# Optimization experiments

Measured on AMD Instinct MI355X. Metric: run time of the kernel, lower is better.

Reference implementation:

```python
import jax, jax.numpy as jnp
import numpy as np

EMB = 512
HEADS = 8

def setup_inputs() -> dict:
    key = jax.random.key(0)
    ks = jax.random.split(key, 9)
    s = 1.0 / np.sqrt(EMB)
    x = jax.random.normal(ks[0], (32, 4096, EMB), dtype=jnp.float32)
    Wq = jax.random.normal(ks[1], (EMB, EMB), dtype=jnp.float32) * s
    bq = jax.random.normal(ks[2], (EMB,), dtype=jnp.float32) * s
    Wk = jax.random.normal(ks[3], (EMB, EMB), dtype=jnp.float32) * s
    bk = jax.random.normal(ks[4], (EMB,), dtype=jnp.float32) * s
    Wv = jax.random.normal(ks[5], (EMB, EMB), dtype=jnp.float32) * s
    bv = jax.random.normal(ks[6], (EMB,), dtype=jnp.float32) * s
    Wo = jax.random.normal(ks[7], (EMB, EMB), dtype=jnp.float32) * s
    bo = jax.random.normal(ks[8], (EMB,), dtype=jnp.float32) * s
    return {"x": x, "Wq": Wq, "bq": bq, "Wk": Wk, "bk": bk,
            "Wv": Wv, "bv": bv, "Wo": Wo, "bo": bo}

def reference(x, Wq, bq, Wk, bk, Wv, bv, Wo, bo):
    b, n, e = x.shape
    h = HEADS
    d = e // h
    scale = jnp.asarray(d ** 0.5, x.dtype)
    # torch Linear: y = x @ W.T + b
    q = (x @ Wq.T + bq).reshape(b, n, h, d)
    k = (x @ Wk.T + bk).reshape(b, n, h, d)
    v = (x @ Wv.T + bv).reshape(b, n, h, d)
    # NOTE: contracts over sequence axis n (faithful to original einsum),
    # producing a (b, h, d, d) feature-feature score matrix.
    qk = jnp.einsum('bnhq,bnhk->bhqk', q, k) / scale
    attn = jax.nn.softmax(qk, axis=-1)  # softmax over head_dim axis
    # dropout is identity at inference
    weighted = jnp.einsum('bhqk,bnhk->bnhq', attn, v).reshape(b, n, e)
    return weighted @ Wo.T + bo
```

## Files before the change

### kernel.cpp

```cpp
#include <hip/hip_runtime.h>
#include <hip/hip_bf16.h>
#include <stdint.h>

#define BATCH 32
#define SEQ   4096
#define EMB   512
#define HEADS 8
#define HD    64
#define SCALE 0.125f

typedef __attribute__((ext_vector_type(8))) short bf16x8;
typedef __attribute__((ext_vector_type(4))) float f32x4;

__device__ __forceinline__ unsigned short f2bf(float f) {
    union { float f; unsigned int u; } v; v.f = f;
    unsigned int u = v.u;
    return (unsigned short)((u + 0x7FFFu + ((u >> 16) & 1u)) >> 16);
}
__device__ __forceinline__ float bf2f(unsigned short h) {
    union { unsigned int u; float f; } v; v.u = ((unsigned int)h) << 16;
    return v.f;
}
__device__ __forceinline__ unsigned int cvtpk(float lo, float hi) {
    unsigned int r;
    asm("v_cvt_pk_bf16_f32 %0, %1, %2" : "=v"(r) : "v"(lo), "v"(hi));
    return r;
}
__device__ __forceinline__ float lo_as_f(unsigned int p) {
    union { unsigned int u; float f; } v; v.u = p << 16; return v.f;
}
__device__ __forceinline__ float hi_as_f(unsigned int p) {
    union { unsigned int u; float f; } v; v.u = p & 0xFFFF0000u; return v.f;
}

#define MFMA16(a, b, c) __builtin_amdgcn_mfma_f32_16x16x32_bf16((a), (b), (c), 0, 0, 0)

union F4 { float4 v; float f[4]; };
struct Regs { F4 a0, a1, a2, a3; };

template <int NCHUNK, bool XBF>
__global__ __launch_bounds__(1024) void k1_gram(const float* __restrict__ x,
                                                float* __restrict__ P,
                                                float* __restrict__ svp,
                                                unsigned short* __restrict__ xbf) {
  constexpr int KC  = SEQ / NCHUNK;
  constexpr int NIT = KC / 32;
  constexpr int NWG = BATCH * 4 * NCHUNK;
  constexpr int PER = NWG / 8;
  const int bid = blockIdx.x;
  const int wk  = (bid & 7) * PER + (bid >> 3);
  const int c   = (NCHUNK == 2) ? (wk & 1) : 0;
  const int tt  = (NCHUNK == 2) ? ((wk >> 1) & 3) : (wk & 3);
  const int b   = (NCHUNK == 2) ? (wk >> 3) : (wk >> 2);
  const int mt = (tt >> 1) & 1, nt = tt & 1;
  const int m0 = mt * 256, n0 = nt * 256;
  const bool diag = (mt == nt);
  const float* __restrict__ xb = x + (size_t)b * SEQ * EMB;
  const int kbeg = c * KC;

  __shared__ unsigned short L[2][64 * 148];
  __shared__ float SR[256][8];

  const int tid  = threadIdx.x;
  const int lane = tid & 63;
  const int wave = tid >> 6;
  const int wr = (wave >> 2) * 64;
  const int wc = (wave & 3) * 64;
  const int er  = lane & 15;
  const int kb8 = (lane >> 4) * 8;

  const int fg   = lane;
  const int kgrp = wave >> 1;
  const bool isB = (wave & 1);
  const int pcol = isB ? n0 : m0;
  const bool active = (!diag) || (!isB);

  f32x4 acc[4][4];
#pragma unroll
  for (int i = 0; i < 4; ++i)
#pragma unroll
    for (int j = 0; j < 4; ++j) acc[i][j] = (f32x4){0.f, 0.f, 0.f, 0.f};

  float sacc[4] = {0.f, 0.f, 0.f, 0.f};

  Regs r0;

  auto loadreg = [&](int t) {
    const float* p = &xb[(size_t)(kbeg + t * 32 + kgrp * 4) * EMB + pcol + fg * 4];
    r0.a0.v = *(const float4*)p;
    r0.a1.v = *(const float4*)(p + EMB);
    r0.a2.v = *(const float4*)(p + 2 * EMB);
    r0.a3.v = *(const float4*)(p + 3 * EMB);
  };

  auto stage = [&](int t) {
    unsigned short* __restrict__ Ld = &L[isB ? 1 : 0][0];
#pragma unroll
    for (int i = 0; i < 4; ++i) {
      uint2 w;
      w.x = cvtpk(r0.a0.f[i], r0.a1.f[i]);
      w.y = cvtpk(r0.a2.f[i], r0.a3.f[i]);
      *(uint2*)&Ld[fg * 148 + i * 36 + kgrp * 4] = w;
    }
    if (diag) {
#pragma unroll
      for (int i = 0; i < 4; ++i)
        sacc[i] += (r0.a0.f[i] + r0.a1.f[i]) + (r0.a2.f[i] + r0.a3.f[i]);
      if (XBF) {
        unsigned short* xp = &xbf[((size_t)b * SEQ + kbeg + t * 32 + kgrp * 4) * EMB + m0 + fg * 4];
        uint2 xr;
        xr.x = cvtpk(r0.a0.f[0], r0.a0.f[1]); xr.y = cvtpk(r0.a0.f[2], r0.a0.f[3]);
        *(uint2*)&xp[0] = xr;
        xr.x = cvtpk(r0.a1.f[0], r0.a1.f[1]); xr.y = cvtpk(r0.a1.f[2], r0.a1.f[3]);
        *(uint2*)&xp[EMB] = xr;
        xr.x = cvtpk(r0.a2.f[0], r0.a2.f[1]); xr.y = cvtpk(r0.a2.f[2], r0.a2.f[3]);
        *(uint2*)&xp[2 * EMB] = xr;
        xr.x = cvtpk(r0.a3.f[0], r0.a3.f[1]); xr.y = cvtpk(r0.a3.f[2], r0.a3.f[3]);
        *(uint2*)&xp[3 * EMB] = xr;
      }
    }
  };

  auto frag = [&](const unsigned short* __restrict__ Ls, int e) -> bf16x8 {
    const int off = (e >> 2) * 148 + (e & 3) * 36 + kb8;
    union { bf16x8 v; uint2 u[2]; } r;
    r.u[0] = *(const uint2*)&Ls[off];
    r.u[1] = *(const uint2*)&Ls[off + 4];
    return r.v;
  };

  if (active) loadreg(0);

  for (int it = 0; it < NIT; ++it) {
    __syncthreads();
    if (active) stage(it);
    __syncthreads();
    if (active && (it + 1 < NIT)) loadreg(it + 1);

    const unsigned short* __restrict__ LAs = &L[0][0];
    const unsigned short* __restrict__ LBs = diag ? LAs : &L[1][0];
    bf16x8 bfr[4];
#pragma unroll
    for (int ns = 0; ns < 4; ++ns) bfr[ns] = frag(LBs, wc + ns * 16 + er);
    {
      bf16x8 a0f = frag(LAs, wr + er);
      bf16x8 a1f = frag(LAs, wr + 16 + er);
#pragma unroll
      for (int ns = 0; ns < 4; ++ns) {
        acc[0][ns] = MFMA16(a0f, bfr[ns], acc[0][ns]);
        acc[1][ns] = MFMA16(a1f, bfr[ns], acc[1][ns]);
      }
    }
    {
      bf16x8 a2f = frag(LAs, wr + 32 + er);
      bf16x8 a3f = frag(LAs, wr + 48 + er);
#pragma unroll
      for (int ns = 0; ns < 4; ++ns) {
        acc[2][ns] = MFMA16(a2f, bfr[ns], acc[2][ns]);
        acc[3][ns] = MFMA16(a3f, bfr[ns], acc[3][ns]);
      }
    }
  }

  float* __restrict__ Pc = P + (size_t)(c * BATCH + b) * EMB * EMB;
#pragma unroll
  for (int ms = 0; ms < 4; ++ms)
#pragma unroll
    for (int ns = 0; ns < 4; ++ns)
#pragma unroll
      for (int r = 0; r < 4; ++r) {
        const int row = m0 + wr + ms * 16 + ((lane >> 4) * 4) + r;
        const int col = n0 + wc + ns * 16 + (lane & 15);
        Pc[(size_t)row * EMB + col] = acc[ms][ns][r];
      }

  if (diag) {
    __syncthreads();
    if (!isB) {
#pragma unroll
      for (int i = 0; i < 4; ++i) SR[fg * 4 + i][kgrp] = sacc[i];
    }
    __syncthreads();
    if (tid < 256) {
      float v = 0.f;
#pragma unroll
      for (int j = 0; j < 8; ++j) v += SR[tid][j];
      svp[(size_t)(c * BATCH + b) * EMB + m0 + tid] = v;
    }
  }
}

template <bool TWO>
__global__ __launch_bounds__(256) void k2a_wqg(const float* __restrict__ Wq,
                                               const float* __restrict__ P,
                                               float* __restrict__ A) {
  const int bid = blockIdx.x;
  const int wk  = (bid & 7) * 64 + (bid >> 3);
  const int b  = wk >> 4;
  const int mt = (wk >> 2) & 3;
  const int nt = wk & 3;
  const int m0 = mt * 128, n0 = nt * 128;
  const float* __restrict__ P0b = P + (size_t)b * EMB * EMB;
  const float* __restrict__ P1b = P + (size_t)(BATCH + b) * EMB * EMB;

  __shared__ unsigned short LA[128][40];
  __shared__ unsigned short LBhi[128][40];
  __shared__ unsigned short LBlo[128][40];

  const int tid  = threadIdx.x;
  const int lane = tid & 63;
  const int wave = tid >> 6;
  const int wr = (wave >> 1) * 64;
  const int wc = (wave & 1) * 64;

  f32x4 acc[4][4];
#pragma unroll
  for (int i = 0; i < 4; ++i)
#pragma unroll
    for (int j = 0; j < 4; ++j) acc[i][j] = (f32x4){0.f, 0.f, 0.f, 0.f};

  const int rA = tid >> 3, fgA = tid & 7;

  for (int k0 = 0; k0 < EMB; k0 += 32) {
    __syncthreads();
#pragma unroll
    for (int it = 0; it < 4; ++it) {
      const int r = rA + it * 32;
      const float4 v = *(const float4*)&Wq[(size_t)(m0 + r) * EMB + k0 + fgA * 4];
      uint2 u; u.x = cvtpk(v.x, v.y); u.y = cvtpk(v.z, v.w);
      *(uint2*)&LA[r][fgA * 4] = u;
    }
#pragma unroll
    for (int it = 0; it < 4; ++it) {
      const int r = rA + it * 32;
      float4 v = *(const float4*)&P0b[(size_t)(n0 + r) * EMB + k0 + fgA * 4];
      if (TWO) {
        const float4 v1 = *(const float4*)&P1b[(size_t)(n0 + r) * EMB + k0 + fgA * 4];
        v.x += v1.x; v.y += v1.y; v.z += v1.z; v.w += v1.w;
      }
      uint2 h; h.x = cvtpk(v.x, v.y); h.y = cvtpk(v.z, v.w);
      uint2 l;
      l.x = cvtpk(v.x - lo_as_f(h.x), v.y - hi_as_f(h.x));
      l.y = cvtpk(v.z - lo_as_f(h.y), v.w - hi_as_f(h.y));
      *(uint2*)&LBhi[r][fgA * 4] = h;
      *(uint2*)&LBlo[r][fgA * 4] = l;
    }
    __syncthreads();
    bf16x8 af[4], bh[4], bl[4];
#pragma unroll
    for (int ms = 0; ms < 4; ++ms)
      af[ms] = *(const bf16x8*)&LA[wr + ms*16 + (lane & 15)][(lane >> 4) * 8];
#pragma unroll
    for (int ns = 0; ns < 4; ++ns) {
      bh[ns] = *(const bf16x8*)&LBhi[wc + ns*16 + (lane & 15)][(lane >> 4) * 8];
      bl[ns] = *(const bf16x8*)&LBlo[wc + ns*16 + (lane & 15)][(lane >> 4) * 8];
    }
#pragma unroll
    for (int ms = 0; ms < 4; ++ms)
#pragma unroll
      for (int ns = 0; ns < 4; ++ns) {
        acc[ms][ns] = MFMA16(af[ms], bh[ns], acc[ms][ns]);
        acc[ms][ns] = MFMA16(af[ms], bl[ns], acc[ms][ns]);
      }
  }

  float* __restrict__ Ab = A + (size_t)b * EMB * EMB;
#pragma unroll
  for (int ms = 0; ms < 4; ++ms)
#pragma unroll
    for (int ns = 0; ns < 4; ++ns)
#pragma unroll
      for (int r = 0; r < 4; ++r) {
        const int row = m0 + wr + ms*16 + ((lane >> 4) * 4) + r;
        const int col = n0 + wc + ns*16 + (lane & 15);
        Ab[(size_t)row * EMB + col] = acc[ms][ns][r];
      }
}

template <int NCHUNK>
__global__ __launch_bounds__(256) void k2b_logits(const float* __restrict__ A,
                                                  const float* __restrict__ Wq,
                                                  const float* __restrict__ Wk,
                                                  const float* __restrict__ bq,
                                                  const float* __restrict__ bk,
                                                  const float* __restrict__ svp,
                                                  unsigned short* __restrict__ attn) {
  const int blk = blockIdx.x;
  const int b = blk >> 3;
  const int h = blk & 7;
  const float* __restrict__ Ab = A + (size_t)b * EMB * EMB + (size_t)h * HD * EMB;

  __shared__ unsigned short LAhi[64][40];
  __shared__ unsigned short LAlo[64][40];
  __shared__ unsigned short LB[64][40];
  __shared__ float U[HD], W[HD];

  const int tid  = threadIdx.x;
  const int lane = tid & 63;
  const int wave = tid >> 6;

  if (tid < 128) {
    const int q = tid & 63;
    const float* __restrict__ wrow = (tid < 64 ? Wq : Wk) + (size_t)(h * HD + q) * EMB;
    float a = 0.f;
    for (int i = 0; i < EMB; i += 4) {
      const float4 wv = *(const float4*)&wrow[i];
      float4 sv = *(const float4*)&svp[(size_t)b * EMB + i];
      if (NCHUNK == 2) {
        const float4 s1 = *(const float4*)&svp[(size_t)(BATCH + b) * EMB + i];
        sv.x += s1.x; sv.y += s1.y; sv.z += s1.z; sv.w += s1.w;
      }
      a += wv.x*sv.x + wv.y*sv.y + wv.z*sv.z + wv.w*sv.w;
    }
    if (tid < 64) U[q] = a; else W[q] = a;
  }

  f32x4 acc[4];
#pragma unroll
  for (int i = 0; i < 4; ++i) acc[i] = (f32x4){0.f, 0.f, 0.f, 0.f};

  const int r8 = tid >> 3, fg8 = tid & 7;

  for (int k0 = 0; k0 < EMB; k0 += 32) {
    __syncthreads();
#pragma unroll
    for (int it = 0; it < 2; ++it) {
      const int r = r8 + it * 32;
      const float4 v = *(const float4*)&Ab[(size_t)r * EMB + k0 + fg8 * 4];
      uint2 h2; h2.x = cvtpk(v.x, v.y); h2.y = cvtpk(v.z, v.w);
      uint2 l2;
      l2.x = cvtpk(v.x - lo_as_f(h2.x), v.y - hi_as_f(h2.x));
      l2.y = cvtpk(v.z - lo_as_f(h2.y), v.w - hi_as_f(h2.y));
      *(ushort4*)&LAhi[r][fg8*4] = *(ushort4*)&h2;
      *(ushort4*)&LAlo[r][fg8*4] = *(ushort4*)&l2;
      const float4 wv = *(const float4*)&Wk[(size_t)(h*HD + r) * EMB + k0 + fg8 * 4];
      uint2 ub; ub.x = cvtpk(wv.x, wv.y); ub.y = cvtpk(wv.z, wv.w);
      *(ushort4*)&LB[r][fg8*4] = *(ushort4*)&ub;
    }
    __syncthreads();
    const bf16x8 ah = *(const bf16x8*)&LAhi[wave*16 + (lane & 15)][(lane >> 4) * 8];
    const bf16x8 al = *(const bf16x8*)&LAlo[wave*16 + (lane & 15)][(lane >> 4) * 8];
#pragma unroll
    for (int ns = 0; ns < 4; ++ns) {
      const bf16x8 bb = *(const bf16x8*)&LB[ns*16 + (lane & 15)][(lane >> 4) * 8];
      acc[ns] = MFMA16(ah, bb, acc[ns]);
      acc[ns] = MFMA16(al, bb, acc[ns]);
    }
  }

  const int colb = lane & 15;
  float bkv[4], wv_[4];
#pragma unroll
  for (int ns = 0; ns < 4; ++ns) {
    bkv[ns] = bk[h*HD + ns*16 + colb];
    wv_[ns] = W[ns*16 + colb];
  }
  unsigned short* __restrict__ ab = attn + (size_t)(b * HEADS + h) * HD * HD;
#pragma unroll
  for (int r = 0; r < 4; ++r) {
    const int row = wave*16 + ((lane >> 4) * 4) + r;
    const float bqv = bq[h*HD + row];
    const float uv  = U[row];
    float vals[4];
#pragma unroll
    for (int ns = 0; ns < 4; ++ns)
      vals[ns] = (acc[ns][r] + uv * bkv[ns] + bqv * wv_[ns] + 4096.f * bqv * bkv[ns]) * SCALE;
    float mx = fmaxf(fmaxf(vals[0], vals[1]), fmaxf(vals[2], vals[3]));
#pragma unroll
    for (int m = 1; m < 16; m <<= 1) mx = fmaxf(mx, __shfl_xor(mx, m));
    float sum = 0.f;
#pragma unroll
    for (int ns = 0; ns < 4; ++ns) { vals[ns] = expf(vals[ns] - mx); sum += vals[ns]; }
#pragma unroll
    for (int m = 1; m < 16; m <<= 1) sum += __shfl_xor(sum, m);
    const float inv = 1.f / sum;
#pragma unroll
    for (int ns = 0; ns < 4; ++ns)
      ab[(size_t)row * HD + ns*16 + colb] = f2bf(vals[ns] * inv);
  }
}

__global__ __launch_bounds__(256) void k3a_c(const float* __restrict__ Wo,
                                             const unsigned short* __restrict__ attn,
                                             unsigned short* __restrict__ C) {
  const int blk = blockIdx.x;
  const int b  = blk >> 5;
  const int h  = (blk >> 2) & 7;
  const int mt = blk & 3;
  const int m0 = mt * 128;

  __shared__ unsigned short LA[128][72];
  __shared__ unsigned short LB[64][72];

  const int tid  = threadIdx.x;
  const int lane = tid & 63;
  const int wave = tid >> 6;

  {
    const int r  = tid >> 4;
    const int fg = tid & 15;
#pragma unroll
    for (int it = 0; it < 8; ++it) {
      const int rr = r + it * 16;
      const float4 v = *(const float4*)&Wo[(size_t)(m0 + rr) * EMB + h*HD + fg * 4];
      uint2 u; u.x = cvtpk(v.x, v.y); u.y = cvtpk(v.z, v.w);
      *(uint2*)&LA[rr][fg * 4] = u;
    }
  }
  {
    const unsigned short* __restrict__ ab = attn + (size_t)(b * HEADS + h) * HD * HD;
#pragma unroll
    for (int it = 0; it < 16; ++it) {
      const int f  = tid + 256 * it;
      const int q  = f >> 6;
      const int kp = f & 63;
      LB[kp][q] = ab[q * HD + kp];
    }
  }
  __syncthreads();

  f32x4 acc[2][4];
#pragma unroll
  for (int i = 0; i < 2; ++i)
#pragma unroll
    for (int j = 0; j < 4; ++j) acc[i][j] = (f32x4){0.f, 0.f, 0.f, 0.f};

#pragma unroll
  for (int kk = 0; kk < 2; ++kk) {
    bf16x8 af[2], bfr[4];
#pragma unroll
    for (int ms = 0; ms < 2; ++ms)
      af[ms] = *(const bf16x8*)&LA[wave*32 + ms*16 + (lane & 15)][kk*32 + (lane >> 4) * 8];
#pragma unroll
    for (int ns = 0; ns < 4; ++ns)
      bfr[ns] = *(const bf16x8*)&LB[ns*16 + (lane & 15)][kk*32 + (lane >> 4) * 8];
#pragma unroll
    for (int ms = 0; ms < 2; ++ms)
#pragma unroll
      for (int ns = 0; ns < 4; ++ns)
        acc[ms][ns] = MFMA16(af[ms], bfr[ns], acc[ms][ns]);
  }

  unsigned short* __restrict__ Cb = C + (size_t)b * EMB * EMB;
#pragma unroll
  for (int ms = 0; ms < 2; ++ms)
#pragma unroll
    for (int ns = 0; ns < 4; ++ns)
#pragma unroll
      for (int r = 0; r < 4; ++r) {
        const int row = m0 + wave*32 + ms*16 + ((lane >> 4) * 4) + r;
        const int col = h*HD + ns*16 + (lane & 15);
        Cb[(size_t)row * EMB + col] = f2bf(acc[ms][ns][r]);
      }
}

__global__ __launch_bounds__(256) void k3b_d(const unsigned short* __restrict__ C,
                                             const float* __restrict__ Wv,
                                             unsigned short* __restrict__ D) {
  const int bid = blockIdx.x;
  const int wk  = (bid & 7) * 64 + (bid >> 3);
  const int b  = wk >> 4;
  const int mt = (wk >> 2) & 3;
  const int nt = wk & 3;
  const int m0 = mt * 128, n0 = nt * 128;
  const unsigned short* __restrict__ Cb = C + (size_t)b * EMB * EMB;

  __shared__ unsigned short LA[128][40];
  __shared__ unsigned short LB[128][40];

  const int tid  = threadIdx.x;
  const int lane = tid & 63;
  const int wave = tid >> 6;
  const int wr = (wave >> 1) * 64;
  const int wc = (wave & 1) * 64;

  f32x4 acc[4][4];
#pragma unroll
  for (int i = 0; i < 4; ++i)
#pragma unroll
    for (int j = 0; j < 4; ++j) acc[i][j] = (f32x4){0.f, 0.f, 0.f, 0.f};

  const int kl = tid >> 5, fgB = tid & 31;
  const int rA = tid >> 3, fgA = tid & 7;

  for (int k0 = 0; k0 < EMB; k0 += 32) {
    __syncthreads();
#pragma unroll
    for (int it = 0; it < 4; ++it) {
      const int r = rA + it * 32;
      *(ushort4*)&LA[r][fgA*4] = *(const ushort4*)&Cb[(size_t)(m0 + r) * EMB + k0 + fgA * 4];
    }
#pragma unroll
    for (int it = 0; it < 4; ++it) {
      const int k = kl + it * 8;
      const float4 v = *(const float4*)&Wv[(size_t)(k0 + k) * EMB + n0 + fgB * 4];
      LB[fgB*4+0][k] = f2bf(v.x);
      LB[fgB*4+1][k] = f2bf(v.y);
      LB[fgB*4+2][k] = f2bf(v.z);
      LB[fgB*4+3][k] = f2bf(v.w);
    }
    __syncthreads();
    bf16x8 af[4], bfr[4];
#pragma unroll
    for (int ms = 0; ms < 4; ++ms)
      af[ms] = *(const bf16x8*)&LA[wr + ms*16 + (lane & 15)][(lane >> 4) * 8];
#pragma unroll
    for (int ns = 0; ns < 4; ++ns)
      bfr[ns] = *(const bf16x8*)&LB[wc + ns*16 + (lane & 15)][(lane >> 4) * 8];
#pragma unroll
    for (int ms = 0; ms < 4; ++ms)
#pragma unroll
      for (int ns = 0; ns < 4; ++ns)
        acc[ms][ns] = MFMA16(af[ms], bfr[ns], acc[ms][ns]);
  }

  unsigned short* __restrict__ Db = D + (size_t)b * EMB * EMB;
#pragma unroll
  for (int ms = 0; ms < 4; ++ms)
#pragma unroll
    for (int ns = 0; ns < 4; ++ns)
#pragma unroll
      for (int r = 0; r < 4; ++r) {
        const int row = m0 + wr + ms*16 + ((lane >> 4) * 4) + r;
        const int col = n0 + wc + ns*16 + (lane & 15);
        Db[(size_t)row * EMB + col] = f2bf(acc[ms][ns][r]);
      }
}

__global__ __launch_bounds__(256) void k3c_e(const unsigned short* __restrict__ C,
                                             const float* __restrict__ bv,
                                             const float* __restrict__ bo,
                                             float* __restrict__ evec) {
  const int blk = blockIdx.x;
  const int b = blk >> 4;
  const int g = blk & 15;
  const int tid  = threadIdx.x;
  const int lane = tid & 63;
  const int wave = tid >> 6;

  __shared__ float BV[EMB];
  for (int i = tid; i < EMB; i += 256) BV[i] = bv[i];
  __syncthreads();

  const unsigned short* __restrict__ Cb = C + (size_t)b * EMB * EMB;
#pragma unroll
  for (int p = 0; p < 8; ++p) {
    const int row = g*32 + wave*8 + p;
    const unsigned short* cr = &Cb[(size_t)row * EMB + lane * 8];
    const float* bvp = &BV[lane * 8];
    ushort4 v0 = *(const ushort4*)&cr[0];
    ushort4 v1 = *(const ushort4*)&cr[4];
    float a = bf2f(v0.x)*bvp[0] + bf2f(v0.y)*bvp[1] + bf2f(v0.z)*bvp[2] + bf2f(v0.w)*bvp[3]
            + bf2f(v1.x)*bvp[4] + bf2f(v1.y)*bvp[5] + bf2f(v1.z)*bvp[6] + bf2f(v1.w)*bvp[7];
#pragma unroll
    for (int m = 1; m < 64; m <<= 1) a += __shfl_xor(a, m);
    if (lane == 0) evec[b * EMB + row] = a + bo[row];
  }
}

template <bool XBF>
__global__ __launch_bounds__(256) void k4_out(const float* __restrict__ x,
                                              const unsigned short* __restrict__ xbf,
                                              const unsigned short* __restrict__ D,
                                              const float* __restrict__ evec,
                                              float* __restrict__ out) {
  const int bid = blockIdx.x;
  const int wk  = (bid & 7) * 512 + (bid >> 3);
  const int b  = wk >> 7;
  const int mt = (wk >> 2) & 31;
  const int nt = wk & 3;
  const int m0 = mt * 128, n0 = nt * 128;
  const float* __restrict__ xb = x + (size_t)b * SEQ * EMB;
  const unsigned short* __restrict__ xbb = xbf + (size_t)b * SEQ * EMB;
  const unsigned short* __restrict__ Db = D + (size_t)b * EMB * EMB;

  __shared__ unsigned short L[2][2][128 * 40];

  const int tid  = threadIdx.x;
  const int lane = tid & 63;
  const int wave = tid >> 6;
  const int wr = (wave >> 1) * 64;
  const int wc = (wave & 1) * 64;

  f32x4 acc[4][4];
#pragma unroll
  for (int i = 0; i < 4; ++i)
#pragma unroll
    for (int j = 0; j < 4; ++j) acc[i][j] = (f32x4){0.f, 0.f, 0.f, 0.f};

  const int rA = tid >> 3, fgA = tid & 7;

  F4 fa[4];
  ushort4 ua[4], ub[4];

  auto loadreg = [&](int k0) {
#pragma unroll
    for (int i = 0; i < 4; ++i) {
      const int r = rA + i * 32;
      if (XBF) ua[i] = *(const ushort4*)&xbb[(size_t)(m0 + r) * EMB + k0 + fgA * 4];
      else     fa[i].v = *(const float4*)&xb[(size_t)(m0 + r) * EMB + k0 + fgA * 4];
      ub[i] = *(const ushort4*)&Db[(size_t)(n0 + r) * EMB + k0 + fgA * 4];
    }
  };
  auto stage = [&](int pb) {
#pragma unroll
    for (int i = 0; i < 4; ++i) {
      const int r = rA + i * 32;
      if (XBF) *(ushort4*)&L[pb][0][r * 40 + fgA * 4] = ua[i];
      else {
        uint2 w; w.x = cvtpk(fa[i].f[0], fa[i].f[1]); w.y = cvtpk(fa[i].f[2], fa[i].f[3]);
        *(uint2*)&L[pb][0][r * 40 + fgA * 4] = w;
      }
      *(ushort4*)&L[pb][1][r * 40 + fgA * 4] = ub[i];
    }
  };

  loadreg(0);
  stage(0);
  __syncthreads();

  for (int t = 0; t < 16; ++t) {
    const int cur = t & 1;
    if (t + 1 < 16) loadreg((t + 1) * 32);

    bf16x8 af[4], bfr[4];
#pragma unroll
    for (int ms = 0; ms < 4; ++ms)
      af[ms] = *(const bf16x8*)&L[cur][0][(wr + ms*16 + (lane & 15)) * 40 + (lane >> 4) * 8];
#pragma unroll
    for (int ns = 0; ns < 4; ++ns)
      bfr[ns] = *(const bf16x8*)&L[cur][1][(wc + ns*16 + (lane & 15)) * 40 + (lane >> 4) * 8];
#pragma unroll
    for (int ms = 0; ms < 4; ++ms)
#pragma unroll
      for (int ns = 0; ns < 4; ++ns)
        acc[ms][ns] = MFMA16(af[ms], bfr[ns], acc[ms][ns]);

    if (t + 1 < 16) stage(cur ^ 1);
    __syncthreads();
  }

#pragma unroll
  for (int ms = 0; ms < 4; ++ms)
#pragma unroll
    for (int ns = 0; ns < 4; ++ns)
#pragma unroll
      for (int r = 0; r < 4; ++r) {
        const int row = m0 + wr + ms*16 + ((lane >> 4) * 4) + r;
        const int col = n0 + wc + ns*16 + (lane & 15);
        out[((size_t)b * SEQ + row) * EMB + col] = acc[ms][ns][r] + evec[b * EMB + col];
      }
}

extern "C" void kernel_launch(void* const* d_in, const int* in_sizes, int n_in,
                              void* d_out, int out_size, void* d_ws, size_t ws_size,
                              hipStream_t stream) {
  (void)in_sizes; (void)n_in; (void)out_size;
  const float* x  = (const float*)d_in[0];
  const float* Wq = (const float*)d_in[1];
  const float* bq = (const float*)d_in[2];
  const float* Wk = (const float*)d_in[3];
  const float* bk = (const float*)d_in[4];
  const float* Wv = (const float*)d_in[5];
  const float* bv = (const float*)d_in[6];
  const float* Wo = (const float*)d_in[7];
  const float* bo = (const float*)d_in[8];
  float* out = (float*)d_out;

  char* ws = (char*)d_ws;
  const size_t MB = (size_t)1 << 20;
  const size_t XBF_BYTES = (size_t)BATCH * SEQ * EMB * 2;
  const size_t NEED2 = XBF_BYTES + 98 * MB + 256 * 1024;
  const size_t NEED1 = XBF_BYTES + 66 * MB + 256 * 1024;

  if (ws_size >= NEED2) {
    unsigned short* xbf  = (unsigned short*)(ws);
    float*          P    = (float*)(ws + XBF_BYTES);
    unsigned short* Cm   = (unsigned short*)(ws + XBF_BYTES);
    unsigned short* Dm   = (unsigned short*)(ws + XBF_BYTES + 16 * MB);
    float*          A    = (float*)(ws + XBF_BYTES + 64 * MB);
    unsigned short* attn = (unsigned short*)(ws + XBF_BYTES + 96 * MB);
    float*          svp  = (float*)(ws + XBF_BYTES + 98 * MB);
    float*          ev   = (float*)(ws + XBF_BYTES + 98 * MB + 192 * 1024);

    hipLaunchKernelGGL((k1_gram<2, true>), dim3(BATCH * 8),  dim3(1024), 0, stream, x, P, svp, xbf);
    hipLaunchKernelGGL((k2a_wqg<true>),    dim3(BATCH * 16), dim3(256), 0, stream, Wq, P, A);
    hipLaunchKernelGGL((k2b_logits<2>),    dim3(BATCH * 8),  dim3(256), 0, stream, A, Wq, Wk, bq, bk, svp, attn);
    hipLaunchKernelGGL(k3a_c,              dim3(BATCH * 32), dim3(256), 0, stream, Wo, attn, Cm);
    hipLaunchKernelGGL(k3b_d,              dim3(BATCH * 16), dim3(256), 0, stream, Cm, Wv, Dm);
    hipLaunchKernelGGL(k3c_e,              dim3(BATCH * 16), dim3(256), 0, stream, Cm, bv, bo, ev);
    hipLaunchKernelGGL((k4_out<true>),     dim3(BATCH * 128), dim3(256), 0, stream, x, xbf, Dm, ev, out);
  } else if (ws_size >= NEED1) {
    unsigned short* xbf  = (unsigned short*)(ws);
    float*          P    = (float*)(ws + XBF_BYTES);
    unsigned short* Cm   = (unsigned short*)(ws + XBF_BYTES);
    unsigned short* Dm   = (unsigned short*)(ws + XBF_BYTES + 16 * MB);
    float*          A    = (float*)(ws + XBF_BYTES + 32 * MB);
    unsigned short* attn = (unsigned short*)(ws + XBF_BYTES + 64 * MB);
    float*          svp  = (float*)(ws + XBF_BYTES + 66 * MB);
    float*          ev   = (float*)(ws + XBF_BYTES + 66 * MB + 192 * 1024);

    hipLaunchKernelGGL((k1_gram<1, true>), dim3(BATCH * 4),  dim3(1024), 0, stream, x, P, svp, xbf);
    hipLaunchKernelGGL((k2a_wqg<false>),   dim3(BATCH * 16), dim3(256), 0, stream, Wq, P, A);
    hipLaunchKernelGGL((k2b_logits<1>),    dim3(BATCH * 8),  dim3(256), 0, stream, A, Wq, Wk, bq, bk, svp, attn);
    hipLaunchKernelGGL(k3a_c,              dim3(BATCH * 32), dim3(256), 0, stream, Wo, attn, Cm);
    hipLaunchKernelGGL(k3b_d,              dim3(BATCH * 16), dim3(256), 0, stream, Cm, Wv, Dm);
    hipLaunchKernelGGL(k3c_e,              dim3(BATCH * 16), dim3(256), 0, stream, Cm, bv, bo, ev);
    hipLaunchKernelGGL((k4_out<true>),     dim3(BATCH * 128), dim3(256), 0, stream, x, xbf, Dm, ev, out);
  } else {
    unsigned short* xbf  = (unsigned short*)(ws);
    float*          P    = (float*)(ws);
    unsigned short* Cm   = (unsigned short*)(ws);
    unsigned short* Dm   = (unsigned short*)(ws + 16 * MB);
    float*          A    = (float*)(ws + 32 * MB);
    unsigned short* attn = (unsigned short*)(ws + 64 * MB);
    float*          svp  = (float*)(ws + 66 * MB);
    float*          ev   = (float*)(ws + 66 * MB + 192 * 1024);

    hipLaunchKernelGGL((k1_gram<1, false>), dim3(BATCH * 4),  dim3(1024), 0, stream, x, P, svp, xbf);
    hipLaunchKernelGGL((k2a_wqg<false>),    dim3(BATCH * 16), dim3(256), 0, stream, Wq, P, A);
    hipLaunchKernelGGL((k2b_logits<1>),     dim3(BATCH * 8),  dim3(256), 0, stream, A, Wq, Wk, bq, bk, svp, attn);
    hipLaunchKernelGGL(k3a_c,               dim3(BATCH * 32), dim3(256), 0, stream, Wo, attn, Cm);
    hipLaunchKernelGGL(k3b_d,               dim3(BATCH * 16), dim3(256), 0, stream, Cm, Wv, Dm);
    hipLaunchKernelGGL(k3c_e,               dim3(BATCH * 16), dim3(256), 0, stream, Cm, bv, bo, ev);
    hipLaunchKernelGGL((k4_out<false>),     dim3(BATCH * 128), dim3(256), 0, stream, x, xbf, Dm, ev, out);
  }
}
```

Before: 398.7 us.

## Enlarge output GEMM tiles to 256x256 with 1024-thread blocks

After: 374.5 us. -6.1%, faster.

```diff
diff --git a/kernel.cpp b/kernel.cpp
--- a/kernel.cpp
+++ b/kernel.cpp
@@ -559,28 +559,33 @@
 }
 
 template <bool XBF>
-__global__ __launch_bounds__(256) void k4_out(const float* __restrict__ x,
-                                              const unsigned short* __restrict__ xbf,
-                                              const unsigned short* __restrict__ D,
-                                              const float* __restrict__ evec,
-                                              float* __restrict__ out) {
+__global__ __launch_bounds__(1024) void k4_out(const float* __restrict__ x,
+                                               const unsigned short* __restrict__ xbf,
+                                               const unsigned short* __restrict__ D,
+                                               const float* __restrict__ evec,
+                                               float* __restrict__ out) {
   const int bid = blockIdx.x;
-  const int wk  = (bid & 7) * 512 + (bid >> 3);
-  const int b  = wk >> 7;
-  const int mt = (wk >> 2) & 31;
-  const int nt = wk & 3;
-  const int m0 = mt * 128, n0 = nt * 128;
+  const int wk  = (bid & 7) * 128 + (bid >> 3);
+  const int b  = wk >> 5;
+  const int mt = (wk >> 1) & 15;
+  const int nt = wk & 1;
+  const int m0 = mt * 256, n0 = nt * 256;
   const float* __restrict__ xb = x + (size_t)b * SEQ * EMB;
   const unsigned short* __restrict__ xbb = xbf + (size_t)b * SEQ * EMB;
   const unsigned short* __restrict__ Db = D + (size_t)b * EMB * EMB;
 
-  __shared__ unsigned short L[2][2][128 * 40];
+  __shared__ unsigned short L[2][256 * 40];
 
   const int tid  = threadIdx.x;
   const int lane = tid & 63;
   const int wave = tid >> 6;
-  const int wr = (wave >> 1) * 64;
-  const int wc = (wave & 1) * 64;
+  const int wr = (wave >> 2) * 64;
+  const int wc = (wave & 3) * 64;
+  const int er  = lane & 15;
+  const int kb8 = (lane >> 4) * 8;
+
+  const int rs = tid >> 2;
+  const int kg = tid & 3;
 
   f32x4 acc[4][4];
 #pragma unroll
@@ -588,57 +593,72 @@
 #pragma unroll
     for (int j = 0; j < 4; ++j) acc[i][j] = (f32x4){0.f, 0.f, 0.f, 0.f};
 
-  const int rA = tid >> 3, fgA = tid & 7;
-
-  F4 fa[4];
-  ushort4 ua[4], ub[4];
+  uint4 ua, ub;
+  F4 fa0, fa1;
 
   auto loadreg = [&](int k0) {
-#pragma unroll
-    for (int i = 0; i < 4; ++i) {
-      const int r = rA + i * 32;
-      if (XBF) ua[i] = *(const ushort4*)&xbb[(size_t)(m0 + r) * EMB + k0 + fgA * 4];
-      else     fa[i].v = *(const float4*)&xb[(size_t)(m0 + r) * EMB + k0 + fgA * 4];
-      ub[i] = *(const ushort4*)&Db[(size_t)(n0 + r) * EMB + k0 + fgA * 4];
-    }
+    if (XBF) {
+      ua = *(const uint4*)&xbb[(size_t)(m0 + rs) * EMB + k0 + kg * 8];
+    } else {
+      fa0.v = *(const float4*)&xb[(size_t)(m0 + rs) * EMB + k0 + kg * 8];
+      fa1.v = *(const float4*)&xb[(size_t)(m0 + rs) * EMB + k0 + kg * 8 + 4];
+    }
+    ub = *(const uint4*)&Db[(size_t)(n0 + rs) * EMB + k0 + kg * 8];
   };
-  auto stage = [&](int pb) {
-#pragma unroll
-    for (int i = 0; i < 4; ++i) {
-      const int r = rA + i * 32;
-      if (XBF) *(ushort4*)&L[pb][0][r * 40 + fgA * 4] = ua[i];
-      else {
-        uint2 w; w.x = cvtpk(fa[i].f[0], fa[i].f[1]); w.y = cvtpk(fa[i].f[2], fa[i].f[3]);
-        *(uint2*)&L[pb][0][r * 40 + fgA * 4] = w;
-      }
-      *(ushort4*)&L[pb][1][r * 40 + fgA * 4] = ub[i];
-    }
+
+  auto stage = [&]() {
+    if (XBF) {
+      *(uint4*)&L[0][rs * 40 + kg * 8] = ua;
+    } else {
+      uint4 w;
+      w.x = cvtpk(fa0.f[0], fa0.f[1]); w.y = cvtpk(fa0.f[2], fa0.f[3]);
+      w.z = cvtpk(fa1.f[0], fa1.f[1]); w.w = cvtpk(fa1.f[2], fa1.f[3]);
+      *(uint4*)&L[0][rs * 40 + kg * 8] = w;
+    }
+    *(uint4*)&L[1][rs * 40 + kg * 8] = ub;
   };
 
+  auto frag = [&](const unsigned short* __restrict__ Ls, int e) -> bf16x8 {
+    return *(const bf16x8*)&Ls[e * 40 + kb8];
+  };
+
   loadreg(0);
-  stage(0);
-  __syncthreads();
-
-  for (int t = 0; t < 16; ++t) {
-    const int cur = t & 1;
-    if (t + 1 < 16) loadreg((t + 1) * 32);
-
-    bf16x8 af[4], bfr[4];
-#pragma unroll
-    for (int ms = 0; ms < 4; ++ms)
-      af[ms] = *(const bf16x8*)&L[cur][0][(wr + ms*16 + (lane & 15)) * 40 + (lane >> 4) * 8];
-#pragma unroll
-    for (int ns = 0; ns < 4; ++ns)
-      bfr[ns] = *(const bf16x8*)&L[cur][1][(wc + ns*16 + (lane & 15)) * 40 + (lane >> 4) * 8];
-#pragma unroll
-    for (int ms = 0; ms < 4; ++ms)
-#pragma unroll
-      for (int ns = 0; ns < 4; ++ns)
-        acc[ms][ns] = MFMA16(af[ms], bfr[ns], acc[ms][ns]);
-
-    if (t + 1 < 16) stage(cur ^ 1);
-    __syncthreads();
-  }
+
+  for (int it = 0; it < 16; ++it) {
+    __syncthreads();
+    stage();
+    __syncthreads();
+    if (it + 1 < 16) loadreg((it + 1) * 32);
+
+    const unsigned short* __restrict__ LAs = &L[0][0];
+    const unsigned short* __restrict__ LBs = &L[1][0];
+    bf16x8 bfr[4];
+#pragma unroll
+    for (int ns = 0; ns < 4; ++ns) bfr[ns] = frag(LBs, wc + ns * 16 + er);
+    {
+      bf16x8 a0f = frag(LAs, wr + er);
+      bf16x8 a1f = frag(LAs, wr + 16 + er);
+#pragma unroll
+      for (int ns = 0; ns < 4; ++ns) {
+        acc[0][ns] = MFMA16(a0f, bfr[ns], acc[0][ns]);
+        acc[1][ns] = MFMA16(a1f, bfr[ns], acc[1][ns]);
+      }
+    }
+    {
+      bf16x8 a2f = frag(LAs, wr + 32 + er);
+      bf16x8 a3f = frag(LAs, wr + 48 + er);
+#pragma unroll
+      for (int ns = 0; ns < 4; ++ns) {
+        acc[2][ns] = MFMA16(a2f, bfr[ns], acc[2][ns]);
+        acc[3][ns] = MFMA16(a3f, bfr[ns], acc[3][ns]);
+      }
+    }
+  }
+
+  float ev4[4];
+#pragma unroll
+  for (int ns = 0; ns < 4; ++ns)
+    ev4[ns] = evec[b * EMB + n0 + wc + ns * 16 + (lane & 15)];
 
 #pragma unroll
   for (int ms = 0; ms < 4; ++ms)
@@ -646,9 +666,9 @@
     for (int ns = 0; ns < 4; ++ns)
 #pragma unroll
       for (int r = 0; r < 4; ++r) {
-        const int row = m0 + wr + ms*16 + ((lane >> 4) * 4) + r;
-        const int col = n0 + wc + ns*16 + (lane & 15);
-        out[((size_t)b * SEQ + row) * EMB + col] = acc[ms][ns][r] + evec[b * EMB + col];
+        const int row = m0 + wr + ms * 16 + ((lane >> 4) * 4) + r;
+        const int col = n0 + wc + ns * 16 + (lane & 15);
+        out[((size_t)b * SEQ + row) * EMB + col] = acc[ms][ns][r] + ev4[ns];
       }
 }
 
@@ -689,7 +709,7 @@
     hipLaunchKernelGGL(k3a_c,              dim3(BATCH * 32), dim3(256), 0, stream, Wo, attn, Cm);
     hipLaunchKernelGGL(k3b_d,              dim3(BATCH * 16), dim3(256), 0, stream, Cm, Wv, Dm);
     hipLaunchKernelGGL(k3c_e,              dim3(BATCH * 16), dim3(256), 0, stream, Cm, bv, bo, ev);
-    hipLaunchKernelGGL((k4_out<true>),     dim3(BATCH * 128), dim3(256), 0, stream, x, xbf, Dm, ev, out);
+    hipLaunchKernelGGL((k4_out<true>),     dim3(BATCH * 32), dim3(1024), 0, stream, x, xbf, Dm, ev, out);
   } else if (ws_size >= NEED1) {
     unsigned short* xbf  = (unsigned short*)(ws);
     float*          P    = (float*)(ws + XBF_BYTES);
@@ -706,7 +726,7 @@
     hipLaunchKernelGGL(k3a_c,              dim3(BATCH * 32), dim3(256), 0, stream, Wo, attn, Cm);
     hipLaunchKernelGGL(k3b_d,              dim3(BATCH * 16), dim3(256), 0, stream, Cm, Wv, Dm);
     hipLaunchKernelGGL(k3c_e,              dim3(BATCH * 16), dim3(256), 0, stream, Cm, bv, bo, ev);
-    hipLaunchKernelGGL((k4_out<true>),     dim3(BATCH * 128), dim3(256), 0, stream, x, xbf, Dm, ev, out);
+    hipLaunchKernelGGL((k4_out<true>),     dim3(BATCH * 32), dim3(1024), 0, stream, x, xbf, Dm, ev, out);
   } else {
     unsigned short* xbf  = (unsigned short*)(ws);
     float*          P    = (float*)(ws);
@@ -723,6 +743,6 @@
     hipLaunchKernelGGL(k3a_c,               dim3(BATCH * 32), dim3(256), 0, stream, Wo, attn, Cm);
     hipLaunchKernelGGL(k3b_d,               dim3(BATCH * 16), dim3(256), 0, stream, Cm, Wv, Dm);
     hipLaunchKernelGGL(k3c_e,               dim3(BATCH * 16), dim3(256), 0, stream, Cm, bv, bo, ev);
-    hipLaunchKernelGGL((k4_out<false>),     dim3(BATCH * 128), dim3(256), 0, stream, x, xbf, Dm, ev, out);
-  }
-}
+    hipLaunchKernelGGL((k4_out<false>),     dim3(BATCH * 32), dim3(1024), 0, stream, x, xbf, Dm, ev, out);
+  }
+}
```
